# Optimization experiments

Hardware: AMD Instinct MI355X
Metric: run time of the kernel (lower is better)

Reference implementation:

```python
import jax, jax.numpy as jnp
import numpy as np

N, E, H = 10000, 80000, 128
NODE_DIM, EDGE_DIM, OUT_DIM, L = 7, 21, 2, 10

def _lin(k, i, o):
    s = 1.0 / np.sqrt(i)
    k1, k2 = jax.random.split(k)
    return (jax.random.uniform(k1, (i, o), jnp.float32, -s, s),
            jax.random.uniform(k2, (o,), jnp.float32, -s, s))

def _mlp_params(k, dims):
    ks = jax.random.split(k, len(dims) - 1)
    Ws, bs = [], []
    for kk, i, o in zip(ks, dims[:-1], dims[1:]):
        W, b = _lin(kk, i, o)
        Ws.append(W); bs.append(b)
    return Ws, bs

def _stack_mlps(k, dims, n):
    ks = jax.random.split(k, n)
    per = [_mlp_params(kk, dims) for kk in ks]
    Ws = [jnp.stack([p[0][j] for p in per]) for j in range(3)]
    bs = [jnp.stack([p[1][j] for p in per]) for j in range(3)]
    return Ws, bs

def mlp3(h, W1, b1, W2, b2, W3, b3):
    h = jax.nn.leaky_relu(h @ W1 + b1)  # slope 0.01 = torch LeakyReLU default
    h = jax.nn.leaky_relu(h @ W2 + b2)
    return h @ W3 + b3

def setup_inputs() -> dict:
    key = jax.random.key(0)
    ks = jax.random.split(key, 10)
    inp = {
        'x_type': jax.random.randint(ks[0], (N,), 0, 2),
        'edge_index': jax.random.randint(ks[1], (2, E), 0, N),
        'edge_attr': jax.random.normal(ks[2], (E, EDGE_DIM), jnp.float32),
        'node_dist': jax.random.uniform(ks[3], (E, 1), jnp.float32),
        'embed_w': jax.random.normal(ks[4], (2, NODE_DIM), jnp.float32),
    }
    niW, nib = _mlp_params(ks[5], [NODE_DIM, H, H, H])
    eiW, eib = _mlp_params(ks[6], [EDGE_DIM, H, H, H])
    noW, nob = _mlp_params(ks[7], [H, H, H, OUT_DIM])
    meW, meb = _stack_mlps(ks[8], [3 * H, H, H, H], L)
    mnW, mnb = _stack_mlps(ks[9], [2 * H, H, H, H], L)
    for pre, Ws, bs in [('ni', niW, nib), ('ei', eiW, eib), ('no', noW, nob),
                        ('me', meW, meb), ('mn', mnW, mnb)]:
        for j in range(3):
            inp[f'{pre}_W{j+1}'] = Ws[j]
            inp[f'{pre}_b{j+1}'] = bs[j]
    return inp

def reference(x_type, edge_index, edge_attr, node_dist, embed_w,
              ni_W1, ni_b1, ni_W2, ni_b2, ni_W3, ni_b3,
              ei_W1, ei_b1, ei_W2, ei_b2, ei_W3, ei_b3,
              no_W1, no_b1, no_W2, no_b2, no_W3, no_b3,
              me_W1, me_b1, me_W2, me_b2, me_W3, me_b3,
              mn_W1, mn_b1, mn_W2, mn_b2, mn_W3, mn_b3):
    n = x_type.shape[0]
    src, dst = edge_index[0], edge_index[1]  # PyG: j = source, i = target
    node = mlp3(embed_w[x_type], ni_W1, ni_b1, ni_W2, ni_b2, ni_W3, ni_b3)
    edge = mlp3(edge_attr, ei_W1, ei_b1, ei_W2, ei_b2, ei_W3, ei_b3)
    for i in range(L):
        # message: cat(x_i, x_j, edge_feature) -> edge MLP
        m = mlp3(jnp.concatenate([node[dst], node[src], edge], axis=-1),
                 me_W1[i], me_b1[i], me_W2[i], me_b2[i], me_W3[i], me_b3[i])
        # aggregate: scatter-sum of node_dist-weighted messages onto targets
        aggr = jax.ops.segment_sum(m * node_dist, dst, num_segments=n)
        node = node + mlp3(jnp.concatenate([node, aggr], axis=-1),
                           mn_W1[i], mn_b1[i], mn_W2[i], mn_b2[i], mn_W3[i], mn_b3[i])
        edge = edge + m
    return mlp3(node, no_W1, no_b1, no_W2, no_b2, no_W3, no_b3)
```

## Files before the change

### kernel.cpp

```cpp
#include <hip/hip_runtime.h>


#define NH  128
#define TPB 256

typedef unsigned short u16;
typedef unsigned int   u32;
using s8v = __attribute__((ext_vector_type(8))) short;
using f4v = __attribute__((ext_vector_type(4))) float;


__device__ __forceinline__ u16 bf_hi(float v) {
  u32 u = __float_as_uint(v);
  return (u16)((u + 0x7FFFu + ((u >> 16) & 1u)) >> 16);
}
__device__ __forceinline__ float bf_f(u16 h) { return __uint_as_float((u32)h << 16); }
__device__ __forceinline__ void split2(float v, u16& h, u16& l) {
  h = bf_hi(v); l = bf_hi(v - bf_f(h));
}
__device__ __forceinline__ void split8(const float* v, s8v& fh, s8v& fl) {
  union { u32 u[4]; s8v s; } H, L;
  #pragma unroll
  for (int i = 0; i < 4; ++i) {
    u16 h0, l0, h1, l1;
    split2(v[2*i], h0, l0); split2(v[2*i+1], h1, l1);
    H.u[i] = (u32)h0 | ((u32)h1 << 16);
    L.u[i] = (u32)l0 | ((u32)l1 << 16);
  }
  fh = H.s; fl = L.s;
}

__device__ __forceinline__ f4v mfma3(s8v ah, s8v al, s8v bh, s8v bl, f4v c) {
  c = __builtin_amdgcn_mfma_f32_16x16x32_bf16(ah, bh, c, 0, 0, 0);
  c = __builtin_amdgcn_mfma_f32_16x16x32_bf16(ah, bl, c, 0, 0, 0);
  c = __builtin_amdgcn_mfma_f32_16x16x32_bf16(al, bh, c, 0, 0, 0);
  return c;
}

__device__ __forceinline__ float lrelu(float v) { return v > 0.f ? v : 0.01f * v; }

__device__ __forceinline__ void pack2(f4v a, u32& w0, u32& w1, u32& v0, u32& v1) {
  u16 h[4], lo[4];
  #pragma unroll
  for (int r = 0; r < 4; ++r) { const float x = lrelu(a[r]); split2(x, h[r], lo[r]); }
  w0 = (u32)h[0]  | ((u32)h[1]  << 16); w1 = (u32)h[2]  | ((u32)h[3]  << 16);
  v0 = (u32)lo[0] | ((u32)lo[1] << 16); v1 = (u32)lo[2] | ((u32)lo[3] << 16);
}

__device__ __forceinline__ void trans_frag(f4v a0, f4v a1, int srcA, int srcB, bool sel1,
                                           s8v& fh, s8v& fl) {
  u32 h00,h01,l00,l01, h10,h11,l10,l11;
  pack2(a0, h00,h01,l00,l01);
  pack2(a1, h10,h11,l10,l11);
  union { u32 u[4]; s8v s; } H, L;
  u32 x, y;
  x = __shfl((int)h00, srcA); y = __shfl((int)h10, srcA); H.u[0] = sel1 ? y : x;
  x = __shfl((int)h01, srcA); y = __shfl((int)h11, srcA); H.u[1] = sel1 ? y : x;
  x = __shfl((int)h00, srcB); y = __shfl((int)h10, srcB); H.u[2] = sel1 ? y : x;
  x = __shfl((int)h01, srcB); y = __shfl((int)h11, srcB); H.u[3] = sel1 ? y : x;
  x = __shfl((int)l00, srcA); y = __shfl((int)l10, srcA); L.u[0] = sel1 ? y : x;
  x = __shfl((int)l01, srcA); y = __shfl((int)l11, srcA); L.u[1] = sel1 ? y : x;
  x = __shfl((int)l00, srcB); y = __shfl((int)l10, srcB); L.u[2] = sel1 ? y : x;
  x = __shfl((int)l01, srcB); y = __shfl((int)l11, srcB); L.u[3] = sel1 ? y : x;
  fh = H.s; fl = L.s;
}


__device__ __forceinline__ void gl_lds16(const void* g, void* l) {
  __builtin_amdgcn_global_load_lds(
      (const __attribute__((address_space(1))) void*)g,
      (__attribute__((address_space(3))) void*)l, 16, 0, 0);
}

__device__ __forceinline__ void stage_async(const u16* __restrict__ base, int KW, int LO,
                                            int col, int w, int l, u16* wb) {
  const int glog8 = ((l & 3) ^ ((l >> 3) & 3)) * 8;
  #pragma unroll
  for (int i = 0; i < 2; ++i) {
    const int t2u = (w * 2 + i) * 64;
    const u16* gp = base + (size_t)((t2u + l) >> 2) * KW + col + glog8;
    gl_lds16(gp,      wb + (size_t)t2u * 8);
    gl_lds16(gp + LO, wb + 4096 + (size_t)t2u * 8);
  }
}

__device__ __forceinline__ void wfrag(const u16* panel, int tt, int c, int gsw, s8v& wh, s8v& wl) {
  const u16* p = panel + (16*tt + c) * 32 + gsw * 8;
  wh = *(const s8v*)p;
  wl = *(const s8v*)(p + 4096);
}

#define ME1_OFF 0
#define ME2_OFF 983040
#define ME3_OFF 1310720
#define MN1_OFF 1638400
#define MN2_OFF 2293760
#define MN3_OFF 2621440
#define WT_TOTAL 2949120
#define PREP_ELEMS 1474560

__global__ void __launch_bounds__(256) k_prep(
    const float* __restrict__ meW1, const float* __restrict__ meW2, const float* __restrict__ meW3,
    const float* __restrict__ mnW1, const float* __restrict__ mnW2, const float* __restrict__ mnW3,
    u16* __restrict__ wt) {
  const int id = blockIdx.x * 256 + threadIdx.x;
  if (id >= PREP_ELEMS) return;
  const int l = id / 147456;
  const int rem = id % 147456;
  const float* src; u16* dh; int K, loc;
  if (rem < 49152)       { loc = rem;          K = 384; src = meW1 + (size_t)l*49152; dh = wt + ME1_OFF + (size_t)l*98304; }
  else if (rem < 65536)  { loc = rem - 49152;  K = 128; src = meW2 + (size_t)l*16384; dh = wt + ME2_OFF + (size_t)l*32768; }
  else if (rem < 81920)  { loc = rem - 65536;  K = 128; src = meW3 + (size_t)l*16384; dh = wt + ME3_OFF + (size_t)l*32768; }
  else if (rem < 114688) { loc = rem - 81920;  K = 256; src = mnW1 + (size_t)l*32768; dh = wt + MN1_OFF + (size_t)l*65536; }
  else if (rem < 131072) { loc = rem - 114688; K = 128; src = mnW2 + (size_t)l*16384; dh = wt + MN2_OFF + (size_t)l*32768; }
  else                   { loc = rem - 131072; K = 128; src = mnW3 + (size_t)l*16384; dh = wt + MN3_OFF + (size_t)l*32768; }
  const int n = loc / K, k = loc % K;
  const float v = src[(size_t)k * NH + n];
  u16 h, lo; split2(v, h, lo);
  dh[(size_t)n * K + k] = h;
  dh[(size_t)NH * K + (size_t)n * K + k] = lo;
}


__global__ void __launch_bounds__(256) k_deg(const int* __restrict__ dst, int* __restrict__ cnt, int E) {
  const int e = blockIdx.x * 256 + threadIdx.x;
  if (e < E) atomicAdd(&cnt[dst[e]], 1);
}

__global__ void __launch_bounds__(256) k_scan(int* __restrict__ cur, int* __restrict__ off, int n, int E) {
  __shared__ int ps[256];
  const int t = threadIdx.x;
  const int chunk = (n + 255) / 256;
  const int b0 = t * chunk;
  int s = 0;
  for (int j = 0; j < chunk; ++j) { const int r = b0 + j; if (r < n) s += cur[r]; }
  ps[t] = s; __syncthreads();
  for (int d = 1; d < 256; d <<= 1) {
    const int v = (t >= d) ? ps[t - d] : 0; __syncthreads();
    ps[t] += v; __syncthreads();
  }
  int run = ps[t] - s;
  for (int j = 0; j < chunk; ++j) {
    const int r = b0 + j;
    if (r < n) { const int d = cur[r]; off[r] = run; cur[r] = run; run += d; }
  }
  if (t == 0) off[n] = E;
}

__global__ void __launch_bounds__(256) k_fill(const int* __restrict__ dst, int* __restrict__ cur,
                                              int* __restrict__ csr, int E) {
  const int e = blockIdx.x * 256 + threadIdx.x;
  if (e < E) { const int p = atomicAdd(&cur[dst[e]], 1); csr[p] = e; }
}


__device__ __forceinline__ int swzB(int c) { return c ^ ((c >> 3) & 1); }
__device__ __forceinline__ void fma8(float* a, float s, const float4 b0, const float4 b1) {
  a[0] += s * b0.x; a[1] += s * b0.y; a[2] += s * b0.z; a[3] += s * b0.w;
  a[4] += s * b1.x; a[5] += s * b1.y; a[6] += s * b1.z; a[7] += s * b1.w;
}

template<int RB>
__device__ __forceinline__ void stage_rows128(
    const float* __restrict__ src, int row_base, int nmax, float* As, int t) {
  const int c = t & 31;
  for (int e = t >> 5; e < RB; e += 8) {
    int r = row_base + e; if (r >= nmax) r = nmax - 1;
    const float4 v = reinterpret_cast<const float4*>(src + (size_t)r * NH)[c];
    reinterpret_cast<float4*>(As)[e * 32 + (c ^ ((e >> 2) & 7))] = v;
  }
}

template<int RB>
__device__ __forceinline__ void stage_smallK(
    const float* __restrict__ src, const int* __restrict__ ridx,
    int row_base, int nmax, int F, float* As, int t) {
  for (int i = t; i < RB * F; i += TPB) {
    const int e = i / F, f = i - e * F;
    int r;
    if (ridx) r = ridx[e];
    else { r = row_base + e; if (r >= nmax) r = nmax - 1; }
    As[e * NH + ((((f >> 2) ^ ((e >> 2) & 7)) << 2) | (f & 3))] = src[(size_t)r * F + f];
  }
}

template<int AR>
__device__ __forceinline__ void init_acc(const float* __restrict__ b, float acc[AR][8], int t) {
  const int o0 = (t >> 4) * 8;
  const float4 c0 = *reinterpret_cast<const float4*>(b + o0);
  const float4 c1 = *reinterpret_cast<const float4*>(b + o0 + 4);
  #pragma unroll
  for (int i = 0; i < AR; ++i) {
    acc[i][0] = c0.x; acc[i][1] = c0.y; acc[i][2] = c0.z; acc[i][3] = c0.w;
    acc[i][4] = c1.x; acc[i][5] = c1.y; acc[i][6] = c1.z; acc[i][7] = c1.w;
  }
}

template<int AR>
__device__ __forceinline__ void gemm_block(
    const float* __restrict__ W, int Kpart,
    const float* As, float* Bs, float acc[AR][8], int t) {
  const int e0  = (t & 15) * AR;
  const int g   = t >> 4;
  const int ob0 = swzB(g * 2) * 4;
  const int ob1 = swzB(g * 2 + 1) * 4;
  int sr[AR];
  #pragma unroll
  for (int i = 0; i < AR; ++i) sr[i] = ((e0 + i) >> 2) & 7;
  for (int sub = 0; sub < Kpart; sub += 32) {
    int kmax = Kpart - sub; if (kmax > 32) kmax = 32;
    __syncthreads();
    {
      const int r  = t >> 3;
      const int cb = (t & 7) * 4;
      if (r < kmax) {
        const float4* s4 = reinterpret_cast<const float4*>(W + (size_t)(sub + r) * NH) + cb;
        #pragma unroll
        for (int j = 0; j < 4; ++j)
          *reinterpret_cast<float4*>(Bs + r * NH + swzB(cb + j) * 4) = s4[j];
      }
    }
    __syncthreads();
    if (kmax == 32) {
      #pragma unroll
      for (int k4 = 0; k4 < 8; ++k4) {
        const int gch = (sub >> 2) + k4;
        float4 aa[AR];
        #pragma unroll
        for (int i = 0; i < AR; ++i)
          aa[i] = reinterpret_cast<const float4*>(As)[(e0 + i) * 32 + (gch ^ sr[i])];
        #pragma unroll
        for (int kk = 0; kk < 4; ++kk) {
          const int k = k4 * 4 + kk;
          const float4 b0 = *reinterpret_cast<const float4*>(Bs + k * NH + ob0);
          const float4 b1 = *reinterpret_cast<const float4*>(Bs + k * NH + ob1);
          #pragma unroll
          for (int i = 0; i < AR; ++i) {
            const float a = (kk == 0) ? aa[i].x : (kk == 1) ? aa[i].y : (kk == 2) ? aa[i].z : aa[i].w;
            fma8(acc[i], a, b0, b1);
          }
        }
      }
    } else {
      for (int k = 0; k < kmax; ++k) {
        const int kk = sub + k;
        const float4 b0 = *reinterpret_cast<const float4*>(Bs + k * NH + ob0);
        const float4 b1 = *reinterpret_cast<const float4*>(Bs + k * NH + ob1);
        #pragma unroll
        for (int i = 0; i < AR; ++i) {
          const float a = As[(e0 + i) * NH + ((((kk >> 2) ^ sr[i]) << 2) | (kk & 3))];
          fma8(acc[i], a, b0, b1);
        }
      }
    }
  }
}

template<int AR, bool ACT>
__device__ __forceinline__ void act_store(float* As, float acc[AR][8], int t) {
  const int e0 = (t & 15) * AR;
  const int g  = t >> 4;
  __syncthreads();
  #pragma unroll
  for (int i = 0; i < AR; ++i) {
    const int r = e0 + i;
    const int s = (r >> 2) & 7;
    float v[8];
    #pragma unroll
    for (int j = 0; j < 8; ++j) v[j] = ACT ? lrelu(acc[i][j]) : acc[i][j];
    float4 w0 = {v[0], v[1], v[2], v[3]};
    float4 w1 = {v[4], v[5], v[6], v[7]};
    reinterpret_cast<float4*>(As + r * NH)[(g * 2)     ^ s] = w0;
    reinterpret_cast<float4*>(As + r * NH)[(g * 2 + 1) ^ s] = w1;
  }
  __syncthreads();
}


__global__ void __launch_bounds__(TPB) k_enc_node(
    const int* __restrict__ xt, const float* __restrict__ embed,
    const float* __restrict__ W1, const float* __restrict__ b1,
    const float* __restrict__ W2, const float* __restrict__ b2,
    const float* __restrict__ W3, const float* __restrict__ b3,
    float* __restrict__ node, int n) {
  constexpr int RB = 32, AR = 2;
  __shared__ float As[RB * NH];
  __shared__ float Bs[32 * NH];
  __shared__ int rid[RB];
  const int t = threadIdx.x;
  const int base = blockIdx.x * RB;
  if (t < RB) { int r = base + t; if (r >= n) r = n - 1; rid[t] = xt[r]; }
  __syncthreads();
  stage_smallK<RB>(embed, rid, 0, 2, 7, As, t);
  float acc[AR][8];
  init_acc<AR>(b1, acc, t);
  gemm_block<AR>(W1, 7, As, Bs, acc, t);
  act_store<AR, true>(As, acc, t);
  init_acc<AR>(b2, acc, t);
  gemm_block<AR>(W2, NH, As, Bs, acc, t);
  act_store<AR, true>(As, acc, t);
  init_acc<AR>(b3, acc, t);
  gemm_block<AR>(W3, NH, As, Bs, acc, t);
  const int e0 = (t & 15) * AR, o0 = (t >> 4) * 8;
  #pragma unroll
  for (int i = 0; i < AR; ++i) {
    const int r = base + e0 + i;
    if (r < n) {
      float4 v0 = {acc[i][0], acc[i][1], acc[i][2], acc[i][3]};
      float4 v1 = {acc[i][4], acc[i][5], acc[i][6], acc[i][7]};
      float4* p = reinterpret_cast<float4*>(node + (size_t)r * NH + o0);
      p[0] = v0; p[1] = v1;
    }
  }
}

__global__ void __launch_bounds__(TPB) k_enc_edge(
    const float* __restrict__ ea,
    const float* __restrict__ W1, const float* __restrict__ b1,
    const float* __restrict__ W2, const float* __restrict__ b2,
    const float* __restrict__ W3, const float* __restrict__ b3,
    float* __restrict__ edge, int nE) {
  constexpr int RB = 64, AR = 4;
  __shared__ float As[RB * NH];
  __shared__ float Bs[32 * NH];
  const int t = threadIdx.x;
  const int base = blockIdx.x * RB;
  stage_smallK<RB>(ea, nullptr, base, nE, 21, As, t);
  float acc[AR][8];
  init_acc<AR>(b1, acc, t);
  gemm_block<AR>(W1, 21, As, Bs, acc, t);
  act_store<AR, true>(As, acc, t);
  init_acc<AR>(b2, acc, t);
  gemm_block<AR>(W2, NH, As, Bs, acc, t);
  act_store<AR, true>(As, acc, t);
  init_acc<AR>(b3, acc, t);
  gemm_block<AR>(W3, NH, As, Bs, acc, t);
  const int e0 = (t & 15) * AR, o0 = (t >> 4) * 8;
  #pragma unroll
  for (int i = 0; i < AR; ++i) {
    const int r = base + e0 + i;
    if (r < nE) {
      float4 v0 = {acc[i][0], acc[i][1], acc[i][2], acc[i][3]};
      float4 v1 = {acc[i][4], acc[i][5], acc[i][6], acc[i][7]};
      float4* p = reinterpret_cast<float4*>(edge + (size_t)r * NH + o0);
      p[0] = v0; p[1] = v1;
    }
  }
}

__global__ void __launch_bounds__(TPB) k_dec(
    const float* __restrict__ node,
    const float* __restrict__ W1, const float* __restrict__ b1,
    const float* __restrict__ W2, const float* __restrict__ b2,
    const float* __restrict__ W3, const float* __restrict__ b3,
    float* __restrict__ out, int n) {
  constexpr int RB = 32, AR = 2;
  __shared__ float As[RB * NH];
  __shared__ float Bs[32 * NH];
  const int t = threadIdx.x;
  const int base = blockIdx.x * RB;
  stage_rows128<RB>(node, base, n, As, t);
  float acc[AR][8];
  init_acc<AR>(b1, acc, t);
  gemm_block<AR>(W1, NH, As, Bs, acc, t);
  act_store<AR, true>(As, acc, t);
  init_acc<AR>(b2, acc, t);
  gemm_block<AR>(W2, NH, As, Bs, acc, t);
  act_store<AR, true>(As, acc, t);
  if (t < RB * 2) {
    const int e = t >> 1, oc = t & 1;
    const int r = base + e;
    if (r < n) {
      const int s = (e >> 2) & 7;
      float sum = b3[oc];
      #pragma unroll 8
      for (int k = 0; k < NH; ++k)
        sum += As[e * NH + ((((k >> 2) ^ s) << 2) | (k & 3))] * W3[k * 2 + oc];
      out[(size_t)r * 2 + oc] = sum;
    }
  }
}

__device__ __forceinline__ void msg_stage(int p, const u16* wt1, const u16* wt2, const u16* wt3,
                                          int w, int l, u16* dst) {
  if (p < 12)      stage_async(wt1, 384, 49152, p * 32, w, l, dst);
  else if (p < 16) stage_async(wt2, 128, 16384, (p - 12) * 32, w, l, dst);
  else             stage_async(wt3, 128, 16384, (p - 16) * 32, w, l, dst);
}

__global__ void __launch_bounds__(TPB) k_msg_mm(
    const int* __restrict__ ei, const float* __restrict__ node,
    float* __restrict__ edge, const float* __restrict__ dist, float* __restrict__ mw,
    const u16* __restrict__ wt1, const u16* __restrict__ wt2, const u16* __restrict__ wt3,
    const float* __restrict__ b1, const float* __restrict__ b2, const float* __restrict__ b3,
    int E) {
  __shared__ u16 wbuf[2][8192];
  const int t = threadIdx.x, w = t >> 6, l = t & 63, c = l & 15, g = l >> 4;
  const int gsw = g ^ ((c >> 1) & 3);
  const int wbase = blockIdx.x * 128 + w * 32;
  int e0 = wbase + c, e1 = wbase + 16 + c;
  if (e0 >= E) e0 = E - 1;
  if (e1 >= E) e1 = E - 1;
  const int sj0 = ei[e0], di0 = ei[E + e0];
  const int sj1 = ei[e1], di1 = ei[E + e1];

  const float* ap0[3] = { node + (size_t)di0 * NH, node + (size_t)sj0 * NH, edge + (size_t)e0 * NH };
  const float* ap1[3] = { node + (size_t)di1 * NH, node + (size_t)sj1 * NH, edge + (size_t)e1 * NH };

  stage_async(wt1, 384, 49152, 0, w, l, wbuf[0]);
  float4 aC0 = *(const float4*)(ap0[0] + g*8);
  float4 aC1 = *(const float4*)(ap0[0] + g*8 + 4);
  float4 aC2 = *(const float4*)(ap1[0] + g*8);
  float4 aC3 = *(const float4*)(ap1[0] + g*8 + 4);

  f4v acc1a[8], acc1b[8];
  #pragma unroll
  for (int tt = 0; tt < 8; ++tt) {
    const float4 bb = *(const float4*)(b1 + 16*tt + 4*g);
    acc1a[tt] = f4v{bb.x, bb.y, bb.z, bb.w};
    acc1b[tt] = acc1a[tt];
  }
  __syncthreads();

  const int srcA = ((g & 1) * 2) * 16 + c, srcB = srcA + 16;
  const bool sel1 = (g >> 1) != 0;
  int cur = 0;

  #pragma unroll
  for (int p = 0; p < 12; ++p) {
    msg_stage(p + 1, wt1, wt2, wt3, w, l, wbuf[cur ^ 1]);
    float4 aN0, aN1, aN2, aN3;
    if (p < 11) {
      const int pt = (p + 1) >> 2, kn = (p + 1) & 3;
      aN0 = *(const float4*)(ap0[pt] + kn*32 + g*8);
      aN1 = *(const float4*)(ap0[pt] + kn*32 + g*8 + 4);
      aN2 = *(const float4*)(ap1[pt] + kn*32 + g*8);
      aN3 = *(const float4*)(ap1[pt] + kn*32 + g*8 + 4);
    }
    s8v h0, lo0, h1, lo1;
    { float v[8];
      *(float4*)v = aC0; *(float4*)(v + 4) = aC1; split8(v, h0, lo0);
      *(float4*)v = aC2; *(float4*)(v + 4) = aC3; split8(v, h1, lo1); }
    const u16* panel = wbuf[cur];
    __builtin_amdgcn_s_setprio(1);
    #pragma unroll
    for (int tt = 0; tt < 8; ++tt) {
      s8v wh, wl; wfrag(panel, tt, c, gsw, wh, wl);
      acc1a[tt] = mfma3(wh, wl, h0, lo0, acc1a[tt]);
      acc1b[tt] = mfma3(wh, wl, h1, lo1, acc1b[tt]);
    }
    __builtin_amdgcn_s_setprio(0);
    __syncthreads();
    cur ^= 1;
    if (p < 11) { aC0 = aN0; aC1 = aN1; aC2 = aN2; aC3 = aN3; }
  }

  f4v acc2a[8], acc2b[8];
  #pragma unroll
  for (int tt = 0; tt < 8; ++tt) {
    const float4 bb = *(const float4*)(b2 + 16*tt + 4*g);
    acc2a[tt] = f4v{bb.x, bb.y, bb.z, bb.w};
    acc2b[tt] = acc2a[tt];
  }
  #pragma unroll
  for (int kc = 0; kc < 4; ++kc) {
    msg_stage(13 + kc, wt1, wt2, wt3, w, l, wbuf[cur ^ 1]);
    s8v h0, lo0, h1, lo1;
    trans_frag(acc1a[2*kc], acc1a[2*kc+1], srcA, srcB, sel1, h0, lo0);
    trans_frag(acc1b[2*kc], acc1b[2*kc+1], srcA, srcB, sel1, h1, lo1);
    const u16* panel = wbuf[cur];
    __builtin_amdgcn_s_setprio(1);
    #pragma unroll
    for (int tt = 0; tt < 8; ++tt) {
      s8v wh, wl; wfrag(panel, tt, c, gsw, wh, wl);
      acc2a[tt] = mfma3(wh, wl, h0, lo0, acc2a[tt]);
      acc2b[tt] = mfma3(wh, wl, h1, lo1, acc2b[tt]);
    }
    __builtin_amdgcn_s_setprio(0);
    __syncthreads();
    cur ^= 1;
  }

  f4v acc3a[8], acc3b[8];
  #pragma unroll
  for (int tt = 0; tt < 8; ++tt) {
    const float bv = b3[16*tt + c];
    acc3a[tt] = f4v{bv, bv, bv, bv};
    acc3b[tt] = acc3a[tt];
  }
  #pragma unroll
  for (int kc = 0; kc < 4; ++kc) {
    if (kc < 3) msg_stage(17 + kc, wt1, wt2, wt3, w, l, wbuf[cur ^ 1]);
    s8v h0, lo0, h1, lo1;
    trans_frag(acc2a[2*kc], acc2a[2*kc+1], srcA, srcB, sel1, h0, lo0);
    trans_frag(acc2b[2*kc], acc2b[2*kc+1], srcA, srcB, sel1, h1, lo1);
    const u16* panel = wbuf[cur];
    __builtin_amdgcn_s_setprio(1);
    #pragma unroll
    for (int tt = 0; tt < 8; ++tt) {
      s8v wh, wl; wfrag(panel, tt, c, gsw, wh, wl);
      acc3a[tt] = mfma3(h0, lo0, wh, wl, acc3a[tt]);
      acc3b[tt] = mfma3(h1, lo1, wh, wl, acc3b[tt]);
    }
    __builtin_amdgcn_s_setprio(0);
    if (kc < 3) { __syncthreads(); cur ^= 1; }
  }
  __syncthreads();

  float* slice = ((float*)&wbuf[0][0]) + w * 2048;
  const int rowr = l >> 2, q = l & 3;
  #pragma unroll
  for (int ch = 0; ch < 2; ++ch) {
    #pragma unroll
    for (int tt = 0; tt < 8; ++tt)
      #pragma unroll
      for (int r = 0; r < 4; ++r) {
        const int row = 4*g + r;
        slice[row*128 + (((tt ^ (row & 7)) << 4) | c)] = ch ? acc3b[tt][r] : acc3a[tt][r];
      }
    const int e = wbase + ch * 16 + rowr;
    if (e < E) {
      const float dw = dist[e];
      float* ep = edge + (size_t)e * NH + q * 32;
      float* mp = mw   + (size_t)e * NH + q * 32;
      #pragma unroll
      for (int j = 0; j < 2; ++j)
        #pragma unroll
        for (int v = 0; v < 4; ++v) {
          const float4 m4 = *(const float4*)&slice[rowr*128 + (((2*q + j) ^ (rowr & 7)) << 4) + v*4];
          float4 x = *(const float4*)(ep + j*16 + v*4);
          x.x += m4.x; x.y += m4.y; x.z += m4.z; x.w += m4.w;
          *(float4*)(ep + j*16 + v*4) = x;
          float4 mm = {m4.x*dw, m4.y*dw, m4.z*dw, m4.w*dw};
          *(float4*)(mp + j*16 + v*4) = mm;
        }
    }
    if (ch == 0) __syncthreads();
  }
}

__device__ __forceinline__ void node_stage(int p, const u16* wt1, const u16* wt2, const u16* wt3,
                                           int w, int l, u16* dst) {
  if (p < 8)       stage_async(wt1, 256, 32768, p * 32, w, l, dst);
  else if (p < 12) stage_async(wt2, 128, 16384, (p - 8) * 32, w, l, dst);
  else             stage_async(wt3, 128, 16384, (p - 12) * 32, w, l, dst);
}

__global__ void __launch_bounds__(TPB) k_node_mm(
    const int* __restrict__ off, const int* __restrict__ csr, const float* __restrict__ mw,
    float* __restrict__ node,
    const u16* __restrict__ wt1, const u16* __restrict__ wt2, const u16* __restrict__ wt3,
    const float* __restrict__ b1, const float* __restrict__ b2, const float* __restrict__ b3,
    int n) {
  __shared__ float ag[64][132];
  __shared__ u16 wbuf[2][8192];
  const int t = threadIdx.x, w = t >> 6, l = t & 63, c = l & 15, g = l >> 4;
  const int gsw = g ^ ((c >> 1) & 3);
  const int base = blockIdx.x * 64;

  node_stage(0, wt1, wt2, wt3, w, l, wbuf[0]);

  int nB = base + 16*w + c; if (nB >= n) nB = n - 1;
  const float* aG = node + (size_t)nB * NH;
  float4 aC0 = *(const float4*)(aG + g*8);
  float4 aC1 = *(const float4*)(aG + g*8 + 4);

  {
    const int r = t >> 2, q = t & 3;
    const int rg = base + r;
    float s[32];
    #pragma unroll
    for (int i = 0; i < 32; ++i) s[i] = 0.f;
    if (rg < n) {
      const int eb = off[rg], ee = off[rg + 1];
      for (int ii = eb; ii < ee; ++ii) {
        const float* mp = mw + (size_t)csr[ii] * NH + q * 32;
        #pragma unroll
        for (int u = 0; u < 8; ++u) {
          const float4 x = *(const float4*)(mp + u * 4);
          s[u*4+0] += x.x; s[u*4+1] += x.y; s[u*4+2] += x.z; s[u*4+3] += x.w;
        }
      }
    }
    #pragma unroll
    for (int u = 0; u < 8; ++u)
      *(float4*)&ag[r][q*32 + u*4] = float4{s[u*4+0], s[u*4+1], s[u*4+2], s[u*4+3]};
  }

  f4v acc1[8];
  #pragma unroll
  for (int tt = 0; tt < 8; ++tt) {
    const float4 bb = *(const float4*)(b1 + 16*tt + 4*g);
    acc1[tt] = f4v{bb.x, bb.y, bb.z, bb.w};
  }
  __syncthreads();

  const float* aL = &ag[16*w + c][0];
  const int srcA = ((g & 1) * 2) * 16 + c, srcB = srcA + 16;
  const bool sel1 = (g >> 1) != 0;
  int cur = 0;

  #pragma unroll
  for (int p = 0; p < 8; ++p) {
    const int part = p >> 2, kc = p & 3;
    node_stage(p + 1, wt1, wt2, wt3, w, l, wbuf[cur ^ 1]);
    float4 aN0, aN1;
    if (p < 3) {
      aN0 = *(const float4*)(aG + (kc + 1)*32 + g*8);
      aN1 = *(const float4*)(aG + (kc + 1)*32 + g*8 + 4);
    }
    s8v h0, lo0;
    if (part == 0) {
      float v[8]; *(float4*)v = aC0; *(float4*)(v + 4) = aC1; split8(v, h0, lo0);
    } else {
      float v[8];
      *(float4*)v       = *(const float4*)(aL + kc*32 + g*8);
      *(float4*)(v + 4) = *(const float4*)(aL + kc*32 + g*8 + 4);
      split8(v, h0, lo0);
    }
    const u16* panel = wbuf[cur];
    __builtin_amdgcn_s_setprio(1);
    #pragma unroll
    for (int tt = 0; tt < 8; ++tt) {
      s8v wh, wl; wfrag(panel, tt, c, gsw, wh, wl);
      acc1[tt] = mfma3(wh, wl, h0, lo0, acc1[tt]);
    }
    __builtin_amdgcn_s_setprio(0);
    __syncthreads();
    cur ^= 1;
    if (p < 3) { aC0 = aN0; aC1 = aN1; }
  }

  f4v acc2[8];
  #pragma unroll
  for (int tt = 0; tt < 8; ++tt) {
    const float4 bb = *(const float4*)(b2 + 16*tt + 4*g);
    acc2[tt] = f4v{bb.x, bb.y, bb.z, bb.w};
  }
  #pragma unroll
  for (int kc = 0; kc < 4; ++kc) {
    node_stage(9 + kc, wt1, wt2, wt3, w, l, wbuf[cur ^ 1]);
    s8v h0, lo0;
    trans_frag(acc1[2*kc], acc1[2*kc+1], srcA, srcB, sel1, h0, lo0);
    const u16* panel = wbuf[cur];
    __builtin_amdgcn_s_setprio(1);
    #pragma unroll
    for (int tt = 0; tt < 8; ++tt) {
      s8v wh, wl; wfrag(panel, tt, c, gsw, wh, wl);
      acc2[tt] = mfma3(wh, wl, h0, lo0, acc2[tt]);
    }
    __builtin_amdgcn_s_setprio(0);
    __syncthreads();
    cur ^= 1;
  }

  f4v acc3[8];
  #pragma unroll
  for (int tt = 0; tt < 8; ++tt) {
    const float bv = b3[16*tt + c];
    acc3[tt] = f4v{bv, bv, bv, bv};
  }
  #pragma unroll
  for (int kc = 0; kc < 4; ++kc) {
    if (kc < 3) node_stage(13 + kc, wt1, wt2, wt3, w, l, wbuf[cur ^ 1]);
    s8v h0, lo0;
    trans_frag(acc2[2*kc], acc2[2*kc+1], srcA, srcB, sel1, h0, lo0);
    const u16* panel = wbuf[cur];
    __builtin_amdgcn_s_setprio(1);
    #pragma unroll
    for (int tt = 0; tt < 8; ++tt) {
      s8v wh, wl; wfrag(panel, tt, c, gsw, wh, wl);
      acc3[tt] = mfma3(h0, lo0, wh, wl, acc3[tt]);
    }
    __builtin_amdgcn_s_setprio(0);
    if (kc < 3) { __syncthreads(); cur ^= 1; }
  }
  __syncthreads();

  float* slice = ((float*)&wbuf[0][0]) + w * 2048;
  #pragma unroll
  for (int tt = 0; tt < 8; ++tt)
    #pragma unroll
    for (int r = 0; r < 4; ++r) {
      const int row = 4*g + r;
      slice[row*128 + (((tt ^ (row & 7)) << 4) | c)] = acc3[tt][r];
    }
  const int rowr = l >> 2, q = l & 3;
  const int e = base + 16*w + rowr;
  if (e < n) {
    float* np = node + (size_t)e * NH + q * 32;
    #pragma unroll
    for (int j = 0; j < 2; ++j)
      #pragma unroll
      for (int v = 0; v < 4; ++v) {
        const float4 m4 = *(const float4*)&slice[rowr*128 + (((2*q + j) ^ (rowr & 7)) << 4) + v*4];
        float4 x = *(const float4*)(np + j*16 + v*4);
        x.x += m4.x; x.y += m4.y; x.z += m4.z; x.w += m4.w;
        *(float4*)(np + j*16 + v*4) = x;
      }
  }
}


extern "C" void kernel_launch(void* const* d_in, const int* in_sizes, int n_in,
                              void* d_out, int out_size, void* d_ws, size_t ws_size,
                              hipStream_t stream) {
  const int n = in_sizes[0];
  const int E = in_sizes[3];
  const int* xt      = (const int*)d_in[0];
  const int* ei      = (const int*)d_in[1];
  const float* eattr = (const float*)d_in[2];
  const float* dist  = (const float*)d_in[3];
  const float* embed = (const float*)d_in[4];
  const float* niW1 = (const float*)d_in[5];  const float* nib1 = (const float*)d_in[6];
  const float* niW2 = (const float*)d_in[7];  const float* nib2 = (const float*)d_in[8];
  const float* niW3 = (const float*)d_in[9];  const float* nib3 = (const float*)d_in[10];
  const float* eiW1 = (const float*)d_in[11]; const float* eib1 = (const float*)d_in[12];
  const float* eiW2 = (const float*)d_in[13]; const float* eib2 = (const float*)d_in[14];
  const float* eiW3 = (const float*)d_in[15]; const float* eib3 = (const float*)d_in[16];
  const float* noW1 = (const float*)d_in[17]; const float* nob1 = (const float*)d_in[18];
  const float* noW2 = (const float*)d_in[19]; const float* nob2 = (const float*)d_in[20];
  const float* noW3 = (const float*)d_in[21]; const float* nob3 = (const float*)d_in[22];
  const float* meW1 = (const float*)d_in[23]; const float* meb1 = (const float*)d_in[24];
  const float* meW2 = (const float*)d_in[25]; const float* meb2 = (const float*)d_in[26];
  const float* meW3 = (const float*)d_in[27]; const float* meb3 = (const float*)d_in[28];
  const float* mnW1 = (const float*)d_in[29]; const float* mnb1 = (const float*)d_in[30];
  const float* mnW2 = (const float*)d_in[31]; const float* mnb2 = (const float*)d_in[32];
  const float* mnW3 = (const float*)d_in[33]; const float* mnb3 = (const float*)d_in[34];

  float* out = (float*)d_out;
  const size_t fn = (size_t)n * NH;
  const size_t fe = (size_t)E * NH;

  float* node = (float*)d_ws;
  float* edge = node + fn;
  float* mw   = edge + fe;
  u16*   wt   = (u16*)(mw + fe);
  int*   off  = (int*)(wt + WT_TOTAL);
  int*   cur  = off + (n + 1);
  int*   csr  = cur + n;

  const int nb32   = (n + 31) / 32;
  const int nb64n  = (n + 63) / 64;
  const int nb64e  = (E + 63) / 64;
  const int nb128e = (E + 127) / 128;

  k_prep<<<(PREP_ELEMS + 255) / 256, 256, 0, stream>>>(meW1, meW2, meW3, mnW1, mnW2, mnW3, wt);

  hipMemsetAsync(cur, 0, (size_t)n * sizeof(int), stream);
  k_deg <<<(E + 255) / 256, 256, 0, stream>>>(ei + E, cur, E);
  k_scan<<<1, 256, 0, stream>>>(cur, off, n, E);
  k_fill<<<(E + 255) / 256, 256, 0, stream>>>(ei + E, cur, csr, E);

  k_enc_node<<<nb32,  TPB, 0, stream>>>(xt, embed, niW1, nib1, niW2, nib2, niW3, nib3, node, n);
  k_enc_edge<<<nb64e, TPB, 0, stream>>>(eattr, eiW1, eib1, eiW2, eib2, eiW3, eib3, edge, E);

  for (int l = 0; l < 10; ++l) {
    k_msg_mm<<<nb128e, TPB, 0, stream>>>(ei, node, edge, dist, mw,
        wt + ME1_OFF + (size_t)l * 98304,
        wt + ME2_OFF + (size_t)l * 32768,
        wt + ME3_OFF + (size_t)l * 32768,
        meb1 + (size_t)l * NH, meb2 + (size_t)l * NH, meb3 + (size_t)l * NH, E);
    k_node_mm<<<nb64n, TPB, 0, stream>>>(off, csr, mw, node,
        wt + MN1_OFF + (size_t)l * 65536,
        wt + MN2_OFF + (size_t)l * 32768,
        wt + MN3_OFF + (size_t)l * 32768,
        mnb1 + (size_t)l * NH, mnb2 + (size_t)l * NH, mnb3 + (size_t)l * NH, n);
  }

  k_dec<<<nb32, TPB, 0, stream>>>(node, noW1, nob1, noW2, nob2, noW3, nob3, out, n);
}
```

Before: 1.678 ms.

## Triple-buffer weight panels with vmcnt-based barriers; halve node-MLP block size

Both the message and node MLP kernels move from double to triple-buffered LDS weight panels, prefetching two panels ahead. The full __syncthreads after each panel is replaced by s_waitcnt vmcnt plus s_barrier, so a wave waits only for the older async loads instead of draining all of them. The node kernel now runs 128-thread blocks over 32 nodes each, giving more blocks. In exchange the kernels use more LDS per block, which may lower occupancy, and the hand-written vmcnt thresholds have to match the exact number of outstanding loads. An unused stage_async_n helper that writes to a null LDS pointer is also added.

Result: slower. 1.769 ms (+5.4%).

```diff
diff --git a/kernel.cpp b/kernel.cpp
--- a/kernel.cpp
+++ b/kernel.cpp
@@ -84,11 +84,51 @@
   }
 }
 
+__device__ __forceinline__ void stage_async_n(const u16* __restrict__ base, int KW, int LO,
+                                              int col, int w, int l, u16* wb) {
+  const int glog8 = ((l & 3) ^ ((l >> 3) & 3)) * 8;
+  #pragma unroll
+  for (int i = 0; i < 4; ++i) {
+    const int t2u = (w * 4 + i) * 64;
+    const u16* gp = base + (size_t)((t2u + l) >> 2) * KW + col + glog8;
+    gl_lds16(gp,      wb + (size_t)t2u * 8);
+    gl_lds16(gp + 4096 + (size_t)0, (void*)0);
+  }
+}
+
+__device__ __forceinline__ void stage_async_node(const u16* __restrict__ base, int KW, int LO,
+                                                 int col, int w, int l, u16* wb) {
+  const int glog8 = ((l & 3) ^ ((l >> 3) & 3)) * 8;
+  #pragma unroll
+  for (int i = 0; i < 4; ++i) {
+    const int t2u = (w * 4 + i) * 64;
+    const u16* gp = base + (size_t)((t2u + l) >> 2) * KW + col + glog8;
+    gl_lds16(gp,      wb + (size_t)t2u * 8);
+    gl_lds16(gp + LO, wb + 4096 + (size_t)t2u * 8);
+  }
+}
+
 __device__ __forceinline__ void wfrag(const u16* panel, int tt, int c, int gsw, s8v& wh, s8v& wl) {
   const u16* p = panel + (16*tt + c) * 32 + gsw * 8;
   wh = *(const s8v*)p;
   wl = *(const s8v*)(p + 4096);
 }
+
+#define PASS_SYNC_MSG(p, LAST) \
+  do { \
+    if ((p) <= (LAST) - 2) { asm volatile("s_waitcnt vmcnt(4)" ::: "memory"); } \
+    else if ((p) == (LAST) - 1) { asm volatile("s_waitcnt vmcnt(0)" ::: "memory"); } \
+    __builtin_amdgcn_s_barrier(); \
+    __builtin_amdgcn_sched_barrier(0); \
+  } while (0)
+
+#define PASS_SYNC_NODE(p, LAST) \
+  do { \
+    if ((p) <= (LAST) - 2) { asm volatile("s_waitcnt vmcnt(8)" ::: "memory"); } \
+    else if ((p) == (LAST) - 1) { asm volatile("s_waitcnt vmcnt(0)" ::: "memory"); } \
+    __builtin_amdgcn_s_barrier(); \
+    __builtin_amdgcn_sched_barrier(0); \
+  } while (0)
 
 #define ME1_OFF 0
 #define ME2_OFF 983040
@@ -394,7 +434,7 @@
     const u16* __restrict__ wt1, const u16* __restrict__ wt2, const u16* __restrict__ wt3,
     const float* __restrict__ b1, const float* __restrict__ b2, const float* __restrict__ b3,
     int E) {
-  __shared__ u16 wbuf[2][8192];
+  __shared__ u16 wbuf[3][8192];
   const int t = threadIdx.x, w = t >> 6, l = t & 63, c = l & 15, g = l >> 4;
   const int gsw = g ^ ((c >> 1) & 3);
   const int wbase = blockIdx.x * 128 + w * 32;
@@ -407,11 +447,12 @@
   const float* ap0[3] = { node + (size_t)di0 * NH, node + (size_t)sj0 * NH, edge + (size_t)e0 * NH };
   const float* ap1[3] = { node + (size_t)di1 * NH, node + (size_t)sj1 * NH, edge + (size_t)e1 * NH };
 
-  stage_async(wt1, 384, 49152, 0, w, l, wbuf[0]);
   float4 aC0 = *(const float4*)(ap0[0] + g*8);
   float4 aC1 = *(const float4*)(ap0[0] + g*8 + 4);
   float4 aC2 = *(const float4*)(ap1[0] + g*8);
   float4 aC3 = *(const float4*)(ap1[0] + g*8 + 4);
+  stage_async(wt1, 384, 49152, 0,  w, l, wbuf[0]);
+  stage_async(wt1, 384, 49152, 32, w, l, wbuf[1]);
 
   f4v acc1a[8], acc1b[8];
   #pragma unroll
@@ -424,11 +465,9 @@
 
   const int srcA = ((g & 1) * 2) * 16 + c, srcB = srcA + 16;
   const bool sel1 = (g >> 1) != 0;
-  int cur = 0;
 
   #pragma unroll
   for (int p = 0; p < 12; ++p) {
-    msg_stage(p + 1, wt1, wt2, wt3, w, l, wbuf[cur ^ 1]);
     float4 aN0, aN1, aN2, aN3;
     if (p < 11) {
       const int pt = (p + 1) >> 2, kn = (p + 1) & 3;
@@ -437,11 +476,12 @@
       aN2 = *(const float4*)(ap1[pt] + kn*32 + g*8);
       aN3 = *(const float4*)(ap1[pt] + kn*32 + g*8 + 4);
     }
+    msg_stage(p + 2, wt1, wt2, wt3, w, l, wbuf[(p + 2) % 3]);
     s8v h0, lo0, h1, lo1;
     { float v[8];
       *(float4*)v = aC0; *(float4*)(v + 4) = aC1; split8(v, h0, lo0);
       *(float4*)v = aC2; *(float4*)(v + 4) = aC3; split8(v, h1, lo1); }
-    const u16* panel = wbuf[cur];
+    const u16* panel = wbuf[p % 3];
     __builtin_amdgcn_s_setprio(1);
     #pragma unroll
     for (int tt = 0; tt < 8; ++tt) {
@@ -450,8 +490,7 @@
       acc1b[tt] = mfma3(wh, wl, h1, lo1, acc1b[tt]);
     }
     __builtin_amdgcn_s_setprio(0);
-    __syncthreads();
-    cur ^= 1;
+    PASS_SYNC_MSG(p, 19);
     if (p < 11) { aC0 = aN0; aC1 = aN1; aC2 = aN2; aC3 = aN3; }
   }
 
@@ -464,11 +503,12 @@
   }
   #pragma unroll
   for (int kc = 0; kc < 4; ++kc) {
-    msg_stage(13 + kc, wt1, wt2, wt3, w, l, wbuf[cur ^ 1]);
+    const int p = 12 + kc;
+    msg_stage(p + 2, wt1, wt2, wt3, w, l, wbuf[(p + 2) % 3]);
     s8v h0, lo0, h1, lo1;
     trans_frag(acc1a[2*kc], acc1a[2*kc+1], srcA, srcB, sel1, h0, lo0);
     trans_frag(acc1b[2*kc], acc1b[2*kc+1], srcA, srcB, sel1, h1, lo1);
-    const u16* panel = wbuf[cur];
+    const u16* panel = wbuf[p % 3];
     __builtin_amdgcn_s_setprio(1);
     #pragma unroll
     for (int tt = 0; tt < 8; ++tt) {
@@ -477,8 +517,7 @@
       acc2b[tt] = mfma3(wh, wl, h1, lo1, acc2b[tt]);
     }
     __builtin_amdgcn_s_setprio(0);
-    __syncthreads();
-    cur ^= 1;
+    PASS_SYNC_MSG(p, 19);
   }
 
   f4v acc3a[8], acc3b[8];
@@ -490,11 +529,12 @@
   }
   #pragma unroll
   for (int kc = 0; kc < 4; ++kc) {
-    if (kc < 3) msg_stage(17 + kc, wt1, wt2, wt3, w, l, wbuf[cur ^ 1]);
+    const int p = 16 + kc;
+    if (kc < 2) msg_stage(p + 2, wt1, wt2, wt3, w, l, wbuf[(p + 2) % 3]);
     s8v h0, lo0, h1, lo1;
     trans_frag(acc2a[2*kc], acc2a[2*kc+1], srcA, srcB, sel1, h0, lo0);
     trans_frag(acc2b[2*kc], acc2b[2*kc+1], srcA, srcB, sel1, h1, lo1);
-    const u16* panel = wbuf[cur];
+    const u16* panel = wbuf[p % 3];
     __builtin_amdgcn_s_setprio(1);
     #pragma unroll
     for (int tt = 0; tt < 8; ++tt) {
@@ -503,7 +543,7 @@
       acc3b[tt] = mfma3(h1, lo1, wh, wl, acc3b[tt]);
     }
     __builtin_amdgcn_s_setprio(0);
-    if (kc < 3) { __syncthreads(); cur ^= 1; }
+    if (p < 19) PASS_SYNC_MSG(p, 19);
   }
   __syncthreads();
 
@@ -541,29 +581,30 @@
 
 __device__ __forceinline__ void node_stage(int p, const u16* wt1, const u16* wt2, const u16* wt3,
                                            int w, int l, u16* dst) {
-  if (p < 8)       stage_async(wt1, 256, 32768, p * 32, w, l, dst);
-  else if (p < 12) stage_async(wt2, 128, 16384, (p - 8) * 32, w, l, dst);
-  else             stage_async(wt3, 128, 16384, (p - 12) * 32, w, l, dst);
-}
-
-__global__ void __launch_bounds__(TPB) k_node_mm(
+  if (p < 8)       stage_async_node(wt1, 256, 32768, p * 32, w, l, dst);
+  else if (p < 12) stage_async_node(wt2, 128, 16384, (p - 8) * 32, w, l, dst);
+  else             stage_async_node(wt3, 128, 16384, (p - 12) * 32, w, l, dst);
+}
+
+__global__ void __launch_bounds__(128) k_node_mm(
     const int* __restrict__ off, const int* __restrict__ csr, const float* __restrict__ mw,
     float* __restrict__ node,
     const u16* __restrict__ wt1, const u16* __restrict__ wt2, const u16* __restrict__ wt3,
     const float* __restrict__ b1, const float* __restrict__ b2, const float* __restrict__ b3,
     int n) {
-  __shared__ float ag[64][132];
-  __shared__ u16 wbuf[2][8192];
+  __shared__ float ag[32][132];
+  __shared__ u16 wbuf[3][8192];
   const int t = threadIdx.x, w = t >> 6, l = t & 63, c = l & 15, g = l >> 4;
   const int gsw = g ^ ((c >> 1) & 3);
-  const int base = blockIdx.x * 64;
-
-  node_stage(0, wt1, wt2, wt3, w, l, wbuf[0]);
+  const int base = blockIdx.x * 32;
 
   int nB = base + 16*w + c; if (nB >= n) nB = n - 1;
   const float* aG = node + (size_t)nB * NH;
   float4 aC0 = *(const float4*)(aG + g*8);
   float4 aC1 = *(const float4*)(aG + g*8 + 4);
+
+  node_stage(0, wt1, wt2, wt3, w, l, wbuf[0]);
+  node_stage(1, wt1, wt2, wt3, w, l, wbuf[1]);
 
   {
     const int r = t >> 2, q = t & 3;
@@ -598,17 +639,16 @@
   const float* aL = &ag[16*w + c][0];
   const int srcA = ((g & 1) * 2) * 16 + c, srcB = srcA + 16;
   const bool sel1 = (g >> 1) != 0;
-  int cur = 0;
 
   #pragma unroll
   for (int p = 0; p < 8; ++p) {
     const int part = p >> 2, kc = p & 3;
-    node_stage(p + 1, wt1, wt2, wt3, w, l, wbuf[cur ^ 1]);
     float4 aN0, aN1;
     if (p < 3) {
       aN0 = *(const float4*)(aG + (kc + 1)*32 + g*8);
       aN1 = *(const float4*)(aG + (kc + 1)*32 + g*8 + 4);
     }
+    node_stage(p + 2, wt1, wt2, wt3, w, l, wbuf[(p + 2) % 3]);
     s8v h0, lo0;
     if (part == 0) {
       float v[8]; *(float4*)v = aC0; *(float4*)(v + 4) = aC1; split8(v, h0, lo0);
@@ -618,7 +658,7 @@
       *(float4*)(v + 4) = *(const float4*)(aL + kc*32 + g*8 + 4);
       split8(v, h0, lo0);
     }
-    const u16* panel = wbuf[cur];
+    const u16* panel = wbuf[p % 3];
     __builtin_amdgcn_s_setprio(1);
     #pragma unroll
     for (int tt = 0; tt < 8; ++tt) {
@@ -626,8 +666,7 @@
       acc1[tt] = mfma3(wh, wl, h0, lo0, acc1[tt]);
     }
     __builtin_amdgcn_s_setprio(0);
-    __syncthreads();
-    cur ^= 1;
+    PASS_SYNC_NODE(p, 15);
     if (p < 3) { aC0 = aN0; aC1 = aN1; }
   }
 
@@ -639,10 +678,11 @@
   }
   #pragma unroll
   for (int kc = 0; kc < 4; ++kc) {
-    node_stage(9 + kc, wt1, wt2, wt3, w, l, wbuf[cur ^ 1]);
+    const int p = 8 + kc;
+    node_stage(p + 2, wt1, wt2, wt3, w, l, wbuf[(p + 2) % 3]);
     s8v h0, lo0;
     trans_frag(acc1[2*kc], acc1[2*kc+1], srcA, srcB, sel1, h0, lo0);
-    const u16* panel = wbuf[cur];
+    const u16* panel = wbuf[p % 3];
     __builtin_amdgcn_s_setprio(1);
     #pragma unroll
     for (int tt = 0; tt < 8; ++tt) {
@@ -650,8 +690,7 @@
       acc2[tt] = mfma3(wh, wl, h0, lo0, acc2[tt]);
     }
     __builtin_amdgcn_s_setprio(0);
-    __syncthreads();
-    cur ^= 1;
+    PASS_SYNC_NODE(p, 15);
   }
 
   f4v acc3[8];
@@ -662,10 +701,11 @@
   }
   #pragma unroll
   for (int kc = 0; kc < 4; ++kc) {
-    if (kc < 3) node_stage(13 + kc, wt1, wt2, wt3, w, l, wbuf[cur ^ 1]);
+    const int p = 12 + kc;
+    if (kc < 2) node_stage(p + 2, wt1, wt2, wt3, w, l, wbuf[(p + 2) % 3]);
     s8v h0, lo0;
     trans_frag(acc2[2*kc], acc2[2*kc+1], srcA, srcB, sel1, h0, lo0);
-    const u16* panel = wbuf[cur];
+    const u16* panel = wbuf[p % 3];
     __builtin_amdgcn_s_setprio(1);
     #pragma unroll
     for (int tt = 0; tt < 8; ++tt) {
@@ -673,7 +713,7 @@
       acc3[tt] = mfma3(h0, lo0, wh, wl, acc3[tt]);
     }
     __builtin_amdgcn_s_setprio(0);
-    if (kc < 3) { __syncthreads(); cur ^= 1; }
+    if (p < 15) PASS_SYNC_NODE(p, 15);
   }
   __syncthreads();
 
@@ -685,6 +725,7 @@
       const int row = 4*g + r;
       slice[row*128 + (((tt ^ (row & 7)) << 4) | c)] = acc3[tt][r];
     }
+  __syncthreads();
   const int rowr = l >> 2, q = l & 3;
   const int e = base + 16*w + rowr;
   if (e < n) {
@@ -741,7 +782,6 @@
   int*   csr  = cur + n;
 
   const int nb32   = (n + 31) / 32;
-  const int nb64n  = (n + 63) / 64;
   const int nb64e  = (E + 63) / 64;
   const int nb128e = (E + 127) / 128;
 
@@ -761,7 +801,7 @@
         wt + ME2_OFF + (size_t)l * 32768,
         wt + ME3_OFF + (size_t)l * 32768,
         meb1 + (size_t)l * NH, meb2 + (size_t)l * NH, meb3 + (size_t)l * NH, E);
-    k_node_mm<<<nb64n, TPB, 0, stream>>>(off, csr, mw, node,
+    k_node_mm<<<nb32, 128, 0, stream>>>(off, csr, mw, node,
         wt + MN1_OFF + (size_t)l * 65536,
         wt + MN2_OFF + (size_t)l * 32768,
         wt + MN3_OFF + (size_t)l * 32768,
```
